# Kernel optimization log

Measured on AMD Instinct MI355X. Metric: run time of the kernel, lower is better.

## Reference

```python
import jax, jax.numpy as jnp
import numpy as np
import math

H, D, E, KD = 8, 128, 128, 16      # n_heads, input_dim, embed_dim, key_dim=val_dim
B, NPICK, NDEL = 16, 250, 250      # batch, pickups, deliveries per instance
G = 1 + NPICK + NDEL               # depot + picks + deliveries


def setup_inputs() -> dict:
    key = jax.random.key(0)
    ks = jax.random.split(key, 10)
    sk = 1.0 / math.sqrt(KD)
    se = 1.0 / math.sqrt(E)
    u = lambda k, shp, s: jax.random.uniform(k, shp, jnp.float32, -s, s)
    return {
        "q": jax.random.normal(ks[0], (B, G, D), jnp.float32),
        "W_query": u(ks[1], (H, D, KD), sk),
        "W_key": u(ks[2], (H, D, KD), sk),
        "W_val": u(ks[3], (H, D, KD), sk),
        "W1_query": u(ks[4], (H, D, KD), sk),
        "W2_query": u(ks[5], (H, D, KD), sk),
        "W3_query": u(ks[6], (H, D, KD), sk),
        "W4_query": u(ks[7], (H, D, KD), sk),
        "W_out": u(ks[8], (H, KD, E), se),
        "n_pick": NPICK,
        "n_delivery": NDEL,
    }


def reference(q, W_query, W_key, W_val, W1_query, W2_query, W3_query, W4_query,
              W_out, n_pick, n_delivery):
    h = q                                   # self-attention (h is None in caller)
    Bq, Gq, Dq = h.shape
    nh = W_query.shape[0]
    kd = W_query.shape[2]
    nf = 1.0 / math.sqrt(kd)
    NEG = jnp.float32(-jnp.inf)

    proj = lambda x, W: jnp.einsum('bnd,hdk->hbnk', x, W)   # (H,B,N,kd)
    scores = lambda Q, K: nf * jnp.einsum('hbqk,hbgk->hbqg', Q, K)
    # torch masked_fill_(x==0, -inf) on the group blocks (padding sentinel)
    zmask = lambda c: jnp.where(c == 0, NEG, c)

    Q = proj(q, W_query)
    K = proj(h, W_key)
    V = proj(h, W_val)
    comp = scores(Q, K)                      # (H,B,G,G)

    # split_embeddings: depot at 0, picks 1..n_pick, deliveries at the end
    hp = h[:, 1:1 + n_pick]                  # (B, n_pick, D)
    hd = h[:, 1 + n_pick:]                   # (B, n_delivery, D)

    Kp, Vp = proj(hp, W_key), proj(hp, W_val)
    Kd, Vd = proj(hd, W_key), proj(hd, W_val)

    c_pp = zmask(scores(proj(hp, W1_query), Kp))  # pick  -> all picks
    c_pd = zmask(scores(proj(hp, W2_query), Kd))  # pick  -> all deliveries
    c_dp = zmask(scores(proj(hd, W3_query), Kp))  # deliv -> all picks
    c_dd = zmask(scores(proj(hd, W4_query), Kd))  # deliv -> all deliveries

    def place(block, row_start):
        # scatter block rows into a (H,B,G,cols) tensor filled with -inf
        full = jnp.full((nh, Bq, Gq, block.shape[3]), NEG, dtype=block.dtype)
        return full.at[:, :, row_start:row_start + block.shape[2], :].set(block)

    add_pp = place(c_pp, 1)
    add_pd = place(c_pd, 1)
    add_dd = place(c_dd, Gq - n_delivery)
    add_dp = place(c_dp, Gq - n_delivery)

    comp_full = jnp.concatenate([comp, add_pp, add_pd, add_dd, add_dp], axis=-1)
    attn = jax.nn.softmax(comp_full, axis=-1)

    g, mp, md = Gq, n_pick, n_delivery
    heads = jnp.einsum('hbqg,hbgv->hbqv', attn[..., :g], V)
    heads = heads + jnp.einsum('hbqp,hbpv->hbqv', attn[..., g:g + mp], Vp)
    heads = heads + jnp.einsum('hbqd,hbdv->hbqv', attn[..., g + mp:g + mp + md], Vd)
    heads = heads + jnp.einsum('hbqd,hbdv->hbqv', attn[..., g + mp + md:g + mp + 2 * md], Vd)
    heads = heads + jnp.einsum('hbqp,hbpv->hbqv', attn[..., g + mp + 2 * md:g + 2 * mp + 2 * md], Vp)

    out = jnp.einsum('hbqv,hve->bqe', heads, W_out)   # (B, G, E)
    return out
```

## Files before the change

kernel.cpp:

```cpp
#include <hip/hip_runtime.h>
#include <math.h>

#define NH 8
#define DIM 128
#define KD 16
#define NB 16
#define NG 501
#define NPK 250
#define QROWS 512
#define QSCALE 0.36067376022224085f

typedef unsigned short ushort_t;
typedef __attribute__((ext_vector_type(8))) short short8v;
typedef __attribute__((ext_vector_type(4))) short short4v;
typedef __attribute__((ext_vector_type(2))) short short2v;
typedef __attribute__((ext_vector_type(4))) float f32x4;

#define MFMA(a, b, c) __builtin_amdgcn_mfma_f32_16x16x32_bf16(a, b, c, 0, 0, 0)

static __device__ __forceinline__ ushort_t f2bf(float x) {
  union { float f; unsigned u; } v; v.f = x;
  unsigned r = v.u + 0x7FFFu + ((v.u >> 16) & 1u);
  return (ushort_t)(r >> 16);
}
static __device__ __forceinline__ float bf2f(ushort_t h) {
  union { unsigned u; float f; } v; v.u = ((unsigned)h) << 16;
  return v.f;
}
static __device__ __forceinline__ unsigned cvtpk(float lo, float hi) {
  unsigned r;
  asm("v_cvt_pk_bf16_f32 %0, %1, %2" : "=v"(r) : "v"(lo), "v"(hi));
  return r;
}

__global__ __launch_bounds__(256) void conv_kernel(
    const float* __restrict__ q, ushort_t* __restrict__ qh,
    ushort_t* __restrict__ ql)
{
  int idx = blockIdx.x * 256 + threadIdx.x;
  int b  = idx >> 13;
  int r  = (idx >> 4) & 511;
  int c8 = (idx & 15) * 8;
  short8v h8 = {0,0,0,0,0,0,0,0}, l8 = {0,0,0,0,0,0,0,0};
  if (r < NG) {
    const float* src = &q[(size_t)(b * NG + r) * DIM + c8];
    float4 a = *(const float4*)src, d = *(const float4*)(src + 4);
    float vals[8] = {a.x, a.y, a.z, a.w, d.x, d.y, d.z, d.w};
#pragma unroll
    for (int j = 0; j < 8; ++j) {
      ushort_t hi = f2bf(vals[j]);
      h8[j] = (short)hi;
      l8[j] = (short)f2bf(vals[j] - bf2f(hi));
    }
  }
  size_t off = (size_t)(b * 512 + r) * DIM + c8;
  *(short8v*)&qh[off] = h8;
  *(short8v*)&ql[off] = l8;
}

__global__ __launch_bounds__(256) void proj_kernel(
    const ushort_t* __restrict__ qh_g, const ushort_t* __restrict__ ql_g,
    const float* __restrict__ wq, const float* __restrict__ wk,
    const float* __restrict__ wv, const float* __restrict__ w1,
    const float* __restrict__ w2, const float* __restrict__ w3,
    const float* __restrict__ w4,
    ushort_t* __restrict__ QcH, ushort_t* __restrict__ QcL,
    ushort_t* __restrict__ QPH, ushort_t* __restrict__ QPL,
    ushort_t* __restrict__ QDH, ushort_t* __restrict__ QDL,
    ushort_t* __restrict__ Kb,  ushort_t* __restrict__ Vt)
{
  const int rc = blockIdx.x, b = blockIdx.y, h = blockIdx.z;
  const int tid = threadIdx.x;
  const int wid = tid >> 6, lane = tid & 63;
  const int lrow = lane & 15, kgrp = lane >> 4;
  const size_t hb = (size_t)h * NB + b;

  const float* Wptr[7] = {wq, wk, wv, w1, w2, w3, w4};
  const int p0 = wid * 2;
  const int p1 = (wid < 3) ? wid * 2 + 1 : -1;

  short8v whf[2][4], wlf[2][4];
#pragma unroll
  for (int slot = 0; slot < 2; ++slot) {
    int p = slot ? p1 : p0;
    if (p < 0) continue;
    const float* W = Wptr[p] + h * 2048 + lrow;
#pragma unroll
    for (int c = 0; c < 4; ++c) {
      short8v hh, ll;
#pragma unroll
      for (int j = 0; j < 8; ++j) {
        float v = W[(c * 32 + kgrp * 8 + j) * 16];
        ushort_t hi = f2bf(v);
        hh[j] = (short)hi;
        ll[j] = (short)f2bf(v - bf2f(hi));
      }
      whf[slot][c] = hh; wlf[slot][c] = ll;
    }
  }

  const f32x4 zero4 = {0.f, 0.f, 0.f, 0.f};

#pragma unroll 1
  for (int iter = 0; iter < 2; ++iter) {
    const int rowbase = rc * 64 + iter * 32;
    short8v qhf[2][4], qlf[2][4];
#pragma unroll
    for (int s = 0; s < 2; ++s)
#pragma unroll
      for (int c = 0; c < 4; ++c) {
        size_t off = (size_t)(b * 512 + rowbase + s * 16 + lrow) * DIM + c * 32 + kgrp * 8;
        qhf[s][c] = *(const short8v*)(qh_g + off);
        qlf[s][c] = *(const short8v*)(ql_g + off);
      }

    f32x4 acc[2][2] = {{zero4, zero4}, {zero4, zero4}};
#pragma unroll
    for (int c = 0; c < 4; ++c)
#pragma unroll
      for (int slot = 0; slot < 2; ++slot) {
        int p = slot ? p1 : p0;
        if (p < 0) continue;
#pragma unroll
        for (int s = 0; s < 2; ++s) {
          if (p == 2) {
            acc[slot][s] = MFMA(whf[slot][c], qlf[s][c], acc[slot][s]);
            acc[slot][s] = MFMA(wlf[slot][c], qhf[s][c], acc[slot][s]);
            acc[slot][s] = MFMA(whf[slot][c], qhf[s][c], acc[slot][s]);
          } else {
            acc[slot][s] = MFMA(qlf[s][c], whf[slot][c], acc[slot][s]);
            acc[slot][s] = MFMA(qhf[s][c], wlf[slot][c], acc[slot][s]);
            acc[slot][s] = MFMA(qhf[s][c], whf[slot][c], acc[slot][s]);
          }
        }
      }

#pragma unroll
    for (int slot = 0; slot < 2; ++slot) {
      int p = slot ? p1 : p0;
      if (p < 0) continue;
#pragma unroll
      for (int s = 0; s < 2; ++s) {
#pragma unroll
        for (int rg = 0; rg < 4; ++rg) {
          float x = acc[slot][s][rg];
          if (p == 2) {
            int v = kgrp * 4 + rg;
            int g = rowbase + s * 16 + lrow;
            Vt[hb * 8192 + (size_t)v * 512 + g] = f2bf(x);
          } else {
            int row = rowbase + s * 16 + kgrp * 4 + rg;
            if (p == 0) {
              float xs = x * QSCALE;
              ushort_t hi = f2bf(xs), lo = f2bf(xs - bf2f(hi));
              size_t off = hb * 8192 + (size_t)row * 16 + lrow;
              QcH[off] = hi; QcL[off] = lo;
            } else if (p == 1) {
              ushort_t hi = f2bf(x), lo = f2bf(x - bf2f(hi));
              size_t off = hb * 16384 + (size_t)row * 32 + lrow;
              Kb[off] = hi; Kb[off + 16] = lo;
            } else {
              bool lowr = (p == 3 || p == 4);
              bool write = lowr ? (row <= NPK) : (row > NPK);
              if (write) {
                float xs = (row == 0) ? 0.f : x * QSCALE;
                ushort_t hi = f2bf(xs), lo = f2bf(xs - bf2f(hi));
                ushort_t* dH = (p == 3 || p == 5) ? QPH : QDH;
                ushort_t* dL = (p == 3 || p == 5) ? QPL : QDL;
                size_t off = hb * 8192 + (size_t)row * 16 + lrow;
                dH[off] = hi; dL[off] = lo;
              }
            }
          }
        }
      }
    }
  }
}

__global__ __launch_bounds__(256, 2) void attn_kernel(
    const ushort_t* __restrict__ QcH, const ushort_t* __restrict__ QcL,
    const ushort_t* __restrict__ QPH, const ushort_t* __restrict__ QPL,
    const ushort_t* __restrict__ QDH, const ushort_t* __restrict__ QDL,
    const ushort_t* __restrict__ Kb,  const ushort_t* __restrict__ Vt,
    ushort_t* __restrict__ HdH, ushort_t* __restrict__ HdL)
{
  __shared__ __align__(16) ushort_t Klds[16384];
  __shared__ __align__(16) ushort_t Vlds[8192];

  const int rt = blockIdx.x, b = blockIdx.y, h = blockIdx.z;
  const int tid = threadIdx.x;
  const int wid = tid >> 6, lane = tid & 63;
  const int lhalf = lane >> 4, lcol = lane & 15;
  const size_t hb = (size_t)h * NB + b;

  const ushort_t* Kg = Kb + hb * (size_t)(QROWS * 32);
  for (int c = tid; c < 2048; c += 256)
    *(short8v*)&Klds[c * 8] = *(const short8v*)(Kg + (size_t)c * 8);

  const ushort_t* Vg = Vt + hb * (size_t)(16 * QROWS);
#pragma unroll
  for (int it = 0; it < 4; ++it) {
    int c = it * 256 + tid;
    int blk = (it * 16) + (c & 15);
    int v = (c >> 4) & 15;
    int grp = blk >> 2, lh = blk & 3;
    short8v val = *(const short8v*)(Vg + (size_t)v * QROWS + blk * 8);
    *(short8v*)&Vlds[((grp * 4 + lh) * 16 + v) * 8] = val;
  }
  __syncthreads();

  const int wrow = rt * 128 + wid * 32;
  short8v qch[2], qcl[2], qph[2], qpl[2], qdh[2], qdl[2];
#pragma unroll
  for (int f = 0; f < 2; ++f) {
    int row = wrow + f * 16 + lcol;
    size_t off = hb * (size_t)(QROWS * 16) + (size_t)row * 16;
    size_t offh = off + (lhalf & 1) * 8;
    qch[f] = *(const short8v*)(QcH + offh);
    qph[f] = *(const short8v*)(QPH + offh);
    qdh[f] = *(const short8v*)(QDH + offh);
    short8v zl = {0,0,0,0,0,0,0,0};
    qcl[f] = zl; qpl[f] = zl; qdl[f] = zl;
    if (lhalf < 2) {
      size_t offl = off + lhalf * 8;
      qcl[f] = *(const short8v*)(QcL + offl);
      qpl[f] = *(const short8v*)(QPL + offl);
      qdl[f] = *(const short8v*)(QDL + offl);
    }
  }

  const f32x4 zero4 = {0.f, 0.f, 0.f, 0.f};
  f32x4 Oacc[2] = {zero4, zero4};
  float lsum[2] = {0.f, 0.f};
  const int srcA = ((lhalf & 1) * 2) * 16 + lcol;
  const int srcB = srcA + 16;
  const bool selhi = (lhalf >= 2);

#pragma unroll 1
  for (int grp = 0; grp < 16; ++grp) {
    float pv[2][2][4];
#pragma unroll
    for (int half = 0; half < 2; ++half) {
      const int ch = grp * 2 + half;
      short8v ka = *(const short8v*)&Klds[((ch * 16 + lcol) * 4 + lhalf) * 8];
#pragma unroll
      for (int qf = 0; qf < 2; ++qf) {
        f32x4 sc = MFMA(ka, qcl[qf], zero4);
        sc = MFMA(ka, qch[qf], sc);
        f32x4 se;
        if (ch == 15) {
          f32x4 sp = MFMA(ka, qpl[qf], zero4); sp = MFMA(ka, qph[qf], sp);
          f32x4 sd = MFMA(ka, qdl[qf], zero4); sd = MFMA(ka, qdh[qf], sd);
#pragma unroll
          for (int rg = 0; rg < 4; ++rg) {
            int key = 240 + lhalf * 4 + rg;
            se[rg] = (key <= NPK) ? sp[rg] : sd[rg];
          }
        } else if (ch <= 14) {
          se = MFMA(ka, qpl[qf], zero4); se = MFMA(ka, qph[qf], se);
        } else {
          se = MFMA(ka, qdl[qf], zero4); se = MFMA(ka, qdh[qf], se);
        }
#pragma unroll
        for (int rg = 0; rg < 4; ++rg) {
          float ec = __builtin_amdgcn_exp2f(sc[rg]);
          float ee = (se[rg] == 0.0f) ? 0.0f : __builtin_amdgcn_exp2f(se[rg]);
          if (ch == 0 && rg == 0) ee = (lhalf == 0) ? 0.0f : ee;
          float pt = ec + ee;
          if (ch == 31) pt = (lhalf * 4 + rg <= 4) ? pt : 0.0f;
          lsum[qf] += pt;
          pv[half][qf][rg] = pt;
        }
      }
    }
#pragma unroll
    for (int qf = 0; qf < 2; ++qf) {
      unsigned a0 = cvtpk(pv[0][qf][0], pv[0][qf][1]);
      unsigned a1 = cvtpk(pv[0][qf][2], pv[0][qf][3]);
      unsigned b0 = cvtpk(pv[1][qf][0], pv[1][qf][1]);
      unsigned b1 = cvtpk(pv[1][qf][2], pv[1][qf][3]);
      unsigned h0A = (unsigned)__shfl((int)a0, srcA);
      unsigned h0B = (unsigned)__shfl((int)a1, srcA);
      unsigned h0C = (unsigned)__shfl((int)a0, srcB);
      unsigned h0D = (unsigned)__shfl((int)a1, srcB);
      unsigned h1A = (unsigned)__shfl((int)b0, srcA);
      unsigned h1B = (unsigned)__shfl((int)b1, srcA);
      unsigned h1C = (unsigned)__shfl((int)b0, srcB);
      unsigned h1D = (unsigned)__shfl((int)b1, srcB);
      union { unsigned u[4]; short8v s; } pb;
      pb.u[0] = selhi ? h1A : h0A;
      pb.u[1] = selhi ? h1B : h0B;
      pb.u[2] = selhi ? h1C : h0C;
      pb.u[3] = selhi ? h1D : h0D;
      short8v va = *(const short8v*)&Vlds[((grp * 4 + lhalf) * 16 + lcol) * 8];
      Oacc[qf] = MFMA(va, pb.s, Oacc[qf]);
    }
  }

#pragma unroll
  for (int qf = 0; qf < 2; ++qf) {
    float l = lsum[qf];
    l += __shfl_xor(l, 16);
    l += __shfl_xor(l, 32);
    float inv = 1.0f / l;
    int row = wrow + qf * 16 + lcol;
    if (row < NG) {
      short4v ph, pl;
#pragma unroll
      for (int rg = 0; rg < 4; ++rg) {
        float o = Oacc[qf][rg] * inv;
        ushort_t hi = f2bf(o);
        ph[rg] = (short)hi;
        pl[rg] = (short)f2bf(o - bf2f(hi));
      }
      size_t off = (hb * 512 + (size_t)row) * 16 + lhalf * 4;
      *(short4v*)&HdH[off] = ph;
      *(short4v*)&HdL[off] = pl;
    }
  }
}

__global__ __launch_bounds__(256) void out_kernel(
    const ushort_t* __restrict__ HdH, const ushort_t* __restrict__ HdL,
    const float* __restrict__ Wout, float* __restrict__ out)
{
  const int eh = blockIdx.x, rt = blockIdx.y, b = blockIdx.z;
  const int tid = threadIdx.x;
  const int wid = tid >> 6, lane = tid & 63;
  const int lrow = lane & 15, kgrp = lane >> 4;
  const int e0 = eh * 64 + wid * 16 + lrow;

  short8v bh[4], bl[4];
#pragma unroll
  for (int c = 0; c < 4; ++c) {
    short8v hh, ll;
#pragma unroll
    for (int j = 0; j < 8; ++j) {
      float v = Wout[(size_t)(c * 32 + kgrp * 8 + j) * 128 + e0];
      ushort_t hi = f2bf(v);
      hh[j] = (short)hi;
      ll[j] = (short)f2bf(v - bf2f(hi));
    }
    bh[c] = hh; bl[c] = ll;
  }

  short8v ah[2][4], al[2][4];
#pragma unroll
  for (int s = 0; s < 2; ++s)
#pragma unroll
    for (int c = 0; c < 4; ++c) {
      int hh = (c * 4 + kgrp) >> 1, kd0 = ((c * 4 + kgrp) & 1) * 8;
      size_t off = ((size_t)(hh * NB + b) * 512 + rt * 32 + s * 16 + lrow) * 16 + kd0;
      ah[s][c] = *(const short8v*)(HdH + off);
      al[s][c] = *(const short8v*)(HdL + off);
    }

  const f32x4 zero4 = {0.f, 0.f, 0.f, 0.f};
  f32x4 acc[2] = {zero4, zero4};
#pragma unroll
  for (int c = 0; c < 4; ++c)
#pragma unroll
    for (int s = 0; s < 2; ++s) {
      acc[s] = MFMA(al[s][c], bh[c], acc[s]);
      acc[s] = MFMA(ah[s][c], bl[c], acc[s]);
      acc[s] = MFMA(ah[s][c], bh[c], acc[s]);
    }

#pragma unroll
  for (int s = 0; s < 2; ++s)
#pragma unroll
    for (int rg = 0; rg < 4; ++rg) {
      int g = rt * 32 + s * 16 + kgrp * 4 + rg;
      if (g < NG) out[((size_t)b * NG + g) * 128 + e0] = acc[s][rg];
    }
}

extern "C" void kernel_launch(void* const* d_in, const int* in_sizes, int n_in,
                              void* d_out, int out_size, void* d_ws, size_t ws_size,
                              hipStream_t stream)
{
  const float* q  = (const float*)d_in[0];
  const float* Wq = (const float*)d_in[1];
  const float* Wk = (const float*)d_in[2];
  const float* Wv = (const float*)d_in[3];
  const float* W1 = (const float*)d_in[4];
  const float* W2 = (const float*)d_in[5];
  const float* W3 = (const float*)d_in[6];
  const float* W4 = (const float*)d_in[7];
  const float* Wo = (const float*)d_in[8];
  float* out = (float*)d_out;

  char* wsb = (char*)d_ws;
  ushort_t* qh_g = (ushort_t*)(wsb + (0u  << 20));
  ushort_t* ql_g = (ushort_t*)(wsb + (2u  << 20));
  ushort_t* QcH  = (ushort_t*)(wsb + (4u  << 20));
  ushort_t* QcL  = (ushort_t*)(wsb + (6u  << 20));
  ushort_t* QPH  = (ushort_t*)(wsb + (8u  << 20));
  ushort_t* QPL  = (ushort_t*)(wsb + (10u << 20));
  ushort_t* QDH  = (ushort_t*)(wsb + (12u << 20));
  ushort_t* QDL  = (ushort_t*)(wsb + (14u << 20));
  ushort_t* Kb   = (ushort_t*)(wsb + (16u << 20));
  ushort_t* Vt   = (ushort_t*)(wsb + (20u << 20));
  ushort_t* HdH  = qh_g;
  ushort_t* HdL  = ql_g;

  conv_kernel<<<dim3(512), 256, 0, stream>>>(q, qh_g, ql_g);
  proj_kernel<<<dim3(8, NB, NH), 256, 0, stream>>>(qh_g, ql_g,
                                                   Wq, Wk, Wv, W1, W2, W3, W4,
                                                   QcH, QcL, QPH, QPL, QDH, QDL, Kb, Vt);
  attn_kernel<<<dim3(4, NB, NH), 256, 0, stream>>>(QcH, QcL, QPH, QPL, QDH, QDL,
                                                   Kb, Vt, HdH, HdL);
  out_kernel<<<dim3(2, 16, NB), 256, 0, stream>>>(HdH, HdL, Wo, out);
}
```

Measured before the change: 129.9 us.

## Fuse four stage kernels into one cooperative persistent kernel with grid syncs

Replaces the four separate launches (convert, project, attention, output) with a single cooperative kernel of 256 blocks of 512 threads that runs all stages and separates them with grid.sync. It also converts the weights to split bf16 hi/lo in a tile-friendly layout during the first stage, so later stages load pre-split fragments. The goal is to remove per-launch overhead and inter-kernel gaps. The cost is lower parallelism per stage (256 blocks), the grid barriers themselves, and more register pressure from the 512-thread blocks. The old multi-kernel path is kept as a fallback.

```diff
diff --git a/kernel.cpp b/kernel.cpp
--- a/kernel.cpp
+++ b/kernel.cpp
@@ -1,5 +1,8 @@
 #include <hip/hip_runtime.h>
+#include <hip/hip_cooperative_groups.h>
 #include <math.h>
+
+namespace cg = cooperative_groups;
 
 #define NH 8
 #define DIM 128
@@ -31,6 +34,357 @@
   unsigned r;
   asm("v_cvt_pk_bf16_f32 %0, %1, %2" : "=v"(r) : "v"(lo), "v"(hi));
   return r;
+}
+
+struct FArgs {
+  const float *q, *wq, *wk, *wv, *w1, *w2, *w3, *w4, *wo;
+  float* out;
+  char* ws;
+};
+
+
+__global__ __launch_bounds__(512, 2) void fused_kernel(FArgs a)
+{
+  __shared__ __align__(16) ushort_t Klds[16384];
+  __shared__ __align__(16) ushort_t Vlds[8192];
+
+  char* wsb = a.ws;
+  ushort_t* qh_g = (ushort_t*)(wsb + (0u  << 20));
+  ushort_t* ql_g = (ushort_t*)(wsb + (2u  << 20));
+  ushort_t* QcH  = (ushort_t*)(wsb + (4u  << 20));
+  ushort_t* QcL  = (ushort_t*)(wsb + (6u  << 20));
+  ushort_t* QPH  = (ushort_t*)(wsb + (8u  << 20));
+  ushort_t* QPL  = (ushort_t*)(wsb + (10u << 20));
+  ushort_t* QDH  = (ushort_t*)(wsb + (12u << 20));
+  ushort_t* QDL  = (ushort_t*)(wsb + (14u << 20));
+  ushort_t* Kb   = (ushort_t*)(wsb + (16u << 20));
+  ushort_t* Vt   = (ushort_t*)(wsb + (20u << 20));
+  ushort_t* Wsh  = (ushort_t*)(wsb + (22u << 20));
+  ushort_t* Wsl  = (ushort_t*)(wsb + (23u << 20));
+  ushort_t* Wosh = (ushort_t*)(wsb + (24u << 20));
+  ushort_t* Wosl = (ushort_t*)(wsb + (25u << 20));
+  ushort_t* HdH  = qh_g;
+  ushort_t* HdL  = ql_g;
+
+  cg::grid_group grid = cg::this_grid();
+  const int tid = threadIdx.x;
+  const int wid = tid >> 6, lane = tid & 63;
+
+  {
+    const int idx = blockIdx.x * 512 + tid;
+    {
+      int b = idx >> 13, r = (idx >> 4) & 511, c8 = (idx & 15) * 8;
+      short8v h8 = {0,0,0,0,0,0,0,0}, l8 = {0,0,0,0,0,0,0,0};
+      if (r < NG) {
+        const float* src = &a.q[(size_t)(b * NG + r) * DIM + c8];
+        float4 x = *(const float4*)src, y = *(const float4*)(src + 4);
+        float vals[8] = {x.x, x.y, x.z, x.w, y.x, y.y, y.z, y.w};
+#pragma unroll
+        for (int j = 0; j < 8; ++j) {
+          ushort_t hi = f2bf(vals[j]);
+          h8[j] = (short)hi;
+          l8[j] = (short)f2bf(vals[j] - bf2f(hi));
+        }
+      }
+      size_t off = (size_t)(b * 512 + r) * DIM + c8;
+      *(short8v*)&qh_g[off] = h8;
+      *(short8v*)&ql_g[off] = l8;
+    }
+    if (idx < 114688) {
+      int p = idx >> 14, rem = idx & 16383;
+      int h = rem >> 11, r2 = rem & 2047;
+      int d = r2 >> 4, lrow = r2 & 15;
+      const float* W = (p == 0) ? a.wq : (p == 1) ? a.wk : (p == 2) ? a.wv :
+                       (p == 3) ? a.w1 : (p == 4) ? a.w2 : (p == 5) ? a.w3 : a.w4;
+      float v = W[h * 2048 + d * 16 + lrow];
+      ushort_t hi = f2bf(v), lo = f2bf(v - bf2f(hi));
+      int c = d >> 5, kg = (d >> 3) & 3, j = d & 7;
+      size_t dst = ((((size_t)(p * 8 + h) * 4 + c) * 4 + kg) * 16 + lrow) * 8 + j;
+      Wsh[dst] = hi; Wsl[dst] = lo;
+    }
+    if (idx < 16384) {
+      int hkd = idx >> 7, e = idx & 127;
+      float v = a.wo[(size_t)hkd * 128 + e];
+      ushort_t hi = f2bf(v), lo = f2bf(v - bf2f(hi));
+      int c = hkd >> 5, kg = (hkd >> 3) & 3, j = hkd & 7;
+      size_t dst = (((size_t)c * 4 + kg) * 128 + e) * 8 + j;
+      Wosh[dst] = hi; Wosl[dst] = lo;
+    }
+  }
+  grid.sync();
+
+  {
+    const int lrow = lane & 15, kgrp = lane >> 4;
+    const int sub = wid >> 2, w4 = wid & 3;
+    const int p0 = w4 * 2;
+    const int p1 = (w4 < 3) ? w4 * 2 + 1 : -1;
+    const f32x4 zero4 = {0.f, 0.f, 0.f, 0.f};
+
+#pragma unroll 1
+    for (int u = 0; u < 2; ++u) {
+      const int unit = (blockIdx.x * 2 + sub) * 2 + u;
+      const int rc = unit & 7, b = (unit >> 3) & 15, h = unit >> 7;
+      const size_t hb = (size_t)h * NB + b;
+
+      short8v whf[2][4], wlf[2][4];
+#pragma unroll
+      for (int slot = 0; slot < 2; ++slot) {
+        int p = slot ? p1 : p0;
+        if (p < 0) continue;
+#pragma unroll
+        for (int c = 0; c < 4; ++c) {
+          size_t off = ((((size_t)(p * 8 + h) * 4 + c) * 4 + kgrp) * 16 + lrow) * 8;
+          whf[slot][c] = *(const short8v*)&Wsh[off];
+          wlf[slot][c] = *(const short8v*)&Wsl[off];
+        }
+      }
+
+#pragma unroll 1
+      for (int iter = 0; iter < 2; ++iter) {
+        const int rowbase = rc * 64 + iter * 32;
+        short8v qhf[2][4], qlf[2][4];
+#pragma unroll
+        for (int s = 0; s < 2; ++s)
+#pragma unroll
+          for (int c = 0; c < 4; ++c) {
+            size_t off = (size_t)(b * 512 + rowbase + s * 16 + lrow) * DIM + c * 32 + kgrp * 8;
+            qhf[s][c] = *(const short8v*)(qh_g + off);
+            qlf[s][c] = *(const short8v*)(ql_g + off);
+          }
+
+        f32x4 acc[2][2] = {{zero4, zero4}, {zero4, zero4}};
+#pragma unroll
+        for (int c = 0; c < 4; ++c)
+#pragma unroll
+          for (int slot = 0; slot < 2; ++slot) {
+            int p = slot ? p1 : p0;
+            if (p < 0) continue;
+#pragma unroll
+            for (int s = 0; s < 2; ++s) {
+              if (p == 2) {
+                acc[slot][s] = MFMA(whf[slot][c], qlf[s][c], acc[slot][s]);
+                acc[slot][s] = MFMA(wlf[slot][c], qhf[s][c], acc[slot][s]);
+                acc[slot][s] = MFMA(whf[slot][c], qhf[s][c], acc[slot][s]);
+              } else {
+                acc[slot][s] = MFMA(qlf[s][c], whf[slot][c], acc[slot][s]);
+                acc[slot][s] = MFMA(qhf[s][c], wlf[slot][c], acc[slot][s]);
+                acc[slot][s] = MFMA(qhf[s][c], whf[slot][c], acc[slot][s]);
+              }
+            }
+          }
+
+#pragma unroll
+        for (int slot = 0; slot < 2; ++slot) {
+          int p = slot ? p1 : p0;
+          if (p < 0) continue;
+#pragma unroll
+          for (int s = 0; s < 2; ++s) {
+#pragma unroll
+            for (int rg = 0; rg < 4; ++rg) {
+              float x = acc[slot][s][rg];
+              if (p == 2) {
+                int v = kgrp * 4 + rg;
+                int g = rowbase + s * 16 + lrow;
+                Vt[hb * 8192 + (size_t)v * 512 + g] = f2bf(x);
+              } else {
+                int row = rowbase + s * 16 + kgrp * 4 + rg;
+                if (p == 0) {
+                  float xs = x * QSCALE;
+                  ushort_t hi = f2bf(xs), lo = f2bf(xs - bf2f(hi));
+                  size_t off = hb * 8192 + (size_t)row * 16 + lrow;
+                  QcH[off] = hi; QcL[off] = lo;
+                } else if (p == 1) {
+                  ushort_t hi = f2bf(x), lo = f2bf(x - bf2f(hi));
+                  size_t off = hb * 16384 + (size_t)row * 32 + lrow;
+                  Kb[off] = hi; Kb[off + 16] = lo;
+                } else {
+                  bool lowr = (p == 3 || p == 4);
+                  bool write = lowr ? (row <= NPK) : (row > NPK);
+                  if (write) {
+                    float xs = (row == 0) ? 0.f : x * QSCALE;
+                    ushort_t hi = f2bf(xs), lo = f2bf(xs - bf2f(hi));
+                    ushort_t* dH = (p == 3 || p == 5) ? QPH : QDH;
+                    ushort_t* dL = (p == 3 || p == 5) ? QPL : QDL;
+                    size_t off = hb * 8192 + (size_t)row * 16 + lrow;
+                    dH[off] = hi; dL[off] = lo;
+                  }
+                }
+              }
+            }
+          }
+        }
+      }
+    }
+  }
+  grid.sync();
+
+  {
+    const int lhalf = lane >> 4, lcol = lane & 15;
+    const int srcA = ((lhalf & 1) * 2) * 16 + lcol;
+    const int srcB = srcA + 16;
+    const bool selhi = (lhalf >= 2);
+    const f32x4 zero4 = {0.f, 0.f, 0.f, 0.f};
+
+#pragma unroll 1
+    for (int tt = 0; tt < 2; ++tt) {
+      const int tile = blockIdx.x * 2 + tt;
+      const int rt = tile & 3, b = (tile >> 2) & 15, h = tile >> 6;
+      const size_t hb = (size_t)h * NB + b;
+
+      const ushort_t* Kg = Kb + hb * (size_t)(QROWS * 32);
+      for (int c = tid; c < 2048; c += 512)
+        *(short8v*)&Klds[c * 8] = *(const short8v*)(Kg + (size_t)c * 8);
+
+      const ushort_t* Vg = Vt + hb * (size_t)(16 * QROWS);
+#pragma unroll
+      for (int it = 0; it < 2; ++it) {
+        int i = it * 512 + tid;
+        int v = (i >> 4) & 15;
+        int blk = (i >> 8) * 16 + (i & 15);
+        int g2 = blk >> 2, lh = blk & 3;
+        short8v val = *(const short8v*)(Vg + (size_t)v * QROWS + blk * 8);
+        *(short8v*)&Vlds[((g2 * 4 + lh) * 16 + v) * 8] = val;
+      }
+      __syncthreads();
+
+      const int wrow = rt * 128 + wid * 16;
+      const int row = wrow + lcol;
+      size_t off = hb * (size_t)(QROWS * 16) + (size_t)row * 16;
+      size_t offh = off + (lhalf & 1) * 8;
+      short8v qch = *(const short8v*)(QcH + offh);
+      short8v qph = *(const short8v*)(QPH + offh);
+      short8v qdh = *(const short8v*)(QDH + offh);
+      short8v qcl = {0,0,0,0,0,0,0,0}, qpl = qcl, qdl = qcl;
+      if (lhalf < 2) {
+        size_t offl = off + lhalf * 8;
+        qcl = *(const short8v*)(QcL + offl);
+        qpl = *(const short8v*)(QPL + offl);
+        qdl = *(const short8v*)(QDL + offl);
+      }
+
+      f32x4 Oacc = zero4;
+      float lsum = 0.f;
+
+#pragma unroll 1
+      for (int grp = 0; grp < 16; ++grp) {
+        float pv[2][4];
+#pragma unroll
+        for (int half = 0; half < 2; ++half) {
+          const int ch = grp * 2 + half;
+          short8v ka = *(const short8v*)&Klds[((ch * 16 + lcol) * 4 + lhalf) * 8];
+          f32x4 sc = MFMA(ka, qcl, zero4);
+          sc = MFMA(ka, qch, sc);
+          f32x4 se;
+          if (ch == 15) {
+            f32x4 sp = MFMA(ka, qpl, zero4); sp = MFMA(ka, qph, sp);
+            f32x4 sd = MFMA(ka, qdl, zero4); sd = MFMA(ka, qdh, sd);
+#pragma unroll
+            for (int rg = 0; rg < 4; ++rg) {
+              int key = 240 + lhalf * 4 + rg;
+              se[rg] = (key <= NPK) ? sp[rg] : sd[rg];
+            }
+          } else if (ch <= 14) {
+            se = MFMA(ka, qpl, zero4); se = MFMA(ka, qph, se);
+          } else {
+            se = MFMA(ka, qdl, zero4); se = MFMA(ka, qdh, se);
+          }
+#pragma unroll
+          for (int rg = 0; rg < 4; ++rg) {
+            float ec = __builtin_amdgcn_exp2f(sc[rg]);
+            float ee = (se[rg] == 0.0f) ? 0.0f : __builtin_amdgcn_exp2f(se[rg]);
+            if (ch == 0 && rg == 0) ee = (lhalf == 0) ? 0.0f : ee;
+            float pt = ec + ee;
+            if (ch == 31) pt = (lhalf * 4 + rg <= 4) ? pt : 0.0f;
+            lsum += pt;
+            pv[half][rg] = pt;
+          }
+        }
+        unsigned a0 = cvtpk(pv[0][0], pv[0][1]);
+        unsigned a1 = cvtpk(pv[0][2], pv[0][3]);
+        unsigned b0 = cvtpk(pv[1][0], pv[1][1]);
+        unsigned b1 = cvtpk(pv[1][2], pv[1][3]);
+        unsigned h0A = (unsigned)__shfl((int)a0, srcA);
+        unsigned h0B = (unsigned)__shfl((int)a1, srcA);
+        unsigned h0C = (unsigned)__shfl((int)a0, srcB);
+        unsigned h0D = (unsigned)__shfl((int)a1, srcB);
+        unsigned h1A = (unsigned)__shfl((int)b0, srcA);
+        unsigned h1B = (unsigned)__shfl((int)b1, srcA);
+        unsigned h1C = (unsigned)__shfl((int)b0, srcB);
+        unsigned h1D = (unsigned)__shfl((int)b1, srcB);
+        union { unsigned u[4]; short8v s; } pb;
+        pb.u[0] = selhi ? h1A : h0A;
+        pb.u[1] = selhi ? h1B : h0B;
+        pb.u[2] = selhi ? h1C : h0C;
+        pb.u[3] = selhi ? h1D : h0D;
+        short8v va = *(const short8v*)&Vlds[((grp * 4 + lhalf) * 16 + lcol) * 8];
+        Oacc = MFMA(va, pb.s, Oacc);
+      }
+
+      float l = lsum;
+      l += __shfl_xor(l, 16);
+      l += __shfl_xor(l, 32);
+      float inv = 1.0f / l;
+      if (row < NG) {
+        short4v ph, pl;
+#pragma unroll
+        for (int rg = 0; rg < 4; ++rg) {
+          float o = Oacc[rg] * inv;
+          ushort_t hi = f2bf(o);
+          ph[rg] = (short)hi;
+          pl[rg] = (short)f2bf(o - bf2f(hi));
+        }
+        size_t doff = (hb * 512 + (size_t)row) * 16 + lhalf * 4;
+        *(short4v*)&HdH[doff] = ph;
+        *(short4v*)&HdL[doff] = pl;
+      }
+      __syncthreads();
+    }
+  }
+  grid.sync();
+
+  {
+    const int rt = blockIdx.x & 15, b = blockIdx.x >> 4;
+    const int lrow = lane & 15, kgrp = lane >> 4;
+    const int e0 = wid * 16 + lrow;
+
+    short8v bh[4], bl[4];
+#pragma unroll
+    for (int c = 0; c < 4; ++c) {
+      size_t off = (((size_t)c * 4 + kgrp) * 128 + e0) * 8;
+      bh[c] = *(const short8v*)&Wosh[off];
+      bl[c] = *(const short8v*)&Wosl[off];
+    }
+
+    short8v ah[2][4], al[2][4];
+#pragma unroll
+    for (int s = 0; s < 2; ++s)
+#pragma unroll
+      for (int c = 0; c < 4; ++c) {
+        int hh = (c * 4 + kgrp) >> 1, kd0 = ((c * 4 + kgrp) & 1) * 8;
+        size_t off = ((size_t)(hh * NB + b) * 512 + rt * 32 + s * 16 + lrow) * 16 + kd0;
+        ah[s][c] = *(const short8v*)(HdH + off);
+        al[s][c] = *(const short8v*)(HdL + off);
+      }
+
+    const f32x4 zero4 = {0.f, 0.f, 0.f, 0.f};
+    f32x4 acc[2] = {zero4, zero4};
+#pragma unroll
+    for (int c = 0; c < 4; ++c)
+#pragma unroll
+      for (int s = 0; s < 2; ++s) {
+        acc[s] = MFMA(al[s][c], bh[c], acc[s]);
+        acc[s] = MFMA(ah[s][c], bl[c], acc[s]);
+        acc[s] = MFMA(ah[s][c], bh[c], acc[s]);
+      }
+
+#pragma unroll
+    for (int s = 0; s < 2; ++s)
+#pragma unroll
+      for (int rg = 0; rg < 4; ++rg) {
+        int g = rt * 32 + s * 16 + kgrp * 4 + rg;
+        if (g < NG) a.out[((size_t)b * NG + g) * 128 + e0] = acc[s][rg];
+      }
+  }
 }
 
 __global__ __launch_bounds__(256) void conv_kernel(
@@ -204,9 +558,9 @@
     int c = it * 256 + tid;
     int blk = (it * 16) + (c & 15);
     int v = (c >> 4) & 15;
-    int grp = blk >> 2, lh = blk & 3;
+    int g2 = blk >> 2, lh = blk & 3;
     short8v val = *(const short8v*)(Vg + (size_t)v * QROWS + blk * 8);
-    *(short8v*)&Vlds[((grp * 4 + lh) * 16 + v) * 8] = val;
+    *(short8v*)&Vlds[((g2 * 4 + lh) * 16 + v) * 8] = val;
   }
   __syncthreads();
 
@@ -380,36 +734,49 @@
                               void* d_out, int out_size, void* d_ws, size_t ws_size,
                               hipStream_t stream)
 {
-  const float* q  = (const float*)d_in[0];
-  const float* Wq = (const float*)d_in[1];
-  const float* Wk = (const float*)d_in[2];
-  const float* Wv = (const float*)d_in[3];
-  const float* W1 = (const float*)d_in[4];
-  const float* W2 = (const float*)d_in[5];
-  const float* W3 = (const float*)d_in[6];
-  const float* W4 = (const float*)d_in[7];
-  const float* Wo = (const float*)d_in[8];
-  float* out = (float*)d_out;
-
-  char* wsb = (char*)d_ws;
-  ushort_t* qh_g = (ushort_t*)(wsb + (0u  << 20));
-  ushort_t* ql_g = (ushort_t*)(wsb + (2u  << 20));
-  ushort_t* QcH  = (ushort_t*)(wsb + (4u  << 20));
-  ushort_t* QcL  = (ushort_t*)(wsb + (6u  << 20));
-  ushort_t* QPH  = (ushort_t*)(wsb + (8u  << 20));
-  ushort_t* QPL  = (ushort_t*)(wsb + (10u << 20));
-  ushort_t* QDH  = (ushort_t*)(wsb + (12u << 20));
-  ushort_t* QDL  = (ushort_t*)(wsb + (14u << 20));
-  ushort_t* Kb   = (ushort_t*)(wsb + (16u << 20));
-  ushort_t* Vt   = (ushort_t*)(wsb + (20u << 20));
-  ushort_t* HdH  = qh_g;
-  ushort_t* HdL  = ql_g;
-
-  conv_kernel<<<dim3(512), 256, 0, stream>>>(q, qh_g, ql_g);
-  proj_kernel<<<dim3(8, NB, NH), 256, 0, stream>>>(qh_g, ql_g,
-                                                   Wq, Wk, Wv, W1, W2, W3, W4,
-                                                   QcH, QcL, QPH, QPL, QDH, QDL, Kb, Vt);
-  attn_kernel<<<dim3(4, NB, NH), 256, 0, stream>>>(QcH, QcL, QPH, QPL, QDH, QDL,
-                                                   Kb, Vt, HdH, HdL);
-  out_kernel<<<dim3(2, 16, NB), 256, 0, stream>>>(HdH, HdL, Wo, out);
-}
+  FArgs a;
+  a.q  = (const float*)d_in[0];
+  a.wq = (const float*)d_in[1];
+  a.wk = (const float*)d_in[2];
+  a.wv = (const float*)d_in[3];
+  a.w1 = (const float*)d_in[4];
+  a.w2 = (const float*)d_in[5];
+  a.w3 = (const float*)d_in[6];
+  a.w4 = (const float*)d_in[7];
+  a.wo = (const float*)d_in[8];
+  a.out = (float*)d_out;
+  a.ws  = (char*)d_ws;
+
+  bool done = false;
+  int nb = 0;
+  hipError_t qe = hipOccupancyMaxActiveBlocksPerMultiprocessor(&nb, fused_kernel, 512, 0);
+  if (qe == hipSuccess && nb >= 1) {
+    void* kp[] = {&a};
+    hipError_t le = hipLaunchCooperativeKernel(fused_kernel, dim3(256), dim3(512), kp, 0, stream);
+    done = (le == hipSuccess);
+  }
+
+  if (!done) {
+    char* wsb = (char*)d_ws;
+    ushort_t* qh_g = (ushort_t*)(wsb + (0u  << 20));
+    ushort_t* ql_g = (ushort_t*)(wsb + (2u  << 20));
+    ushort_t* QcH  = (ushort_t*)(wsb + (4u  << 20));
+    ushort_t* QcL  = (ushort_t*)(wsb + (6u  << 20));
+    ushort_t* QPH  = (ushort_t*)(wsb + (8u  << 20));
+    ushort_t* QPL  = (ushort_t*)(wsb + (10u << 20));
+    ushort_t* QDH  = (ushort_t*)(wsb + (12u << 20));
+    ushort_t* QDL  = (ushort_t*)(wsb + (14u << 20));
+    ushort_t* Kb   = (ushort_t*)(wsb + (16u << 20));
+    ushort_t* Vt   = (ushort_t*)(wsb + (20u << 20));
+    ushort_t* HdH  = qh_g;
+    ushort_t* HdL  = ql_g;
+
+    conv_kernel<<<dim3(512), 256, 0, stream>>>(a.q, qh_g, ql_g);
+    proj_kernel<<<dim3(8, NB, NH), 256, 0, stream>>>(qh_g, ql_g,
+                                                     a.wq, a.wk, a.wv, a.w1, a.w2, a.w3, a.w4,
+                                                     QcH, QcL, QPH, QPL, QDH, QDL, Kb, Vt);
+    attn_kernel<<<dim3(4, NB, NH), 256, 0, stream>>>(QcH, QcL, QPH, QPL, QDH, QDL,
+                                                     Kb, Vt, HdH, HdL);
+    out_kernel<<<dim3(2, 16, NB), 256, 0, stream>>>(HdH, HdL, a.wo, out_size ? (float*)d_out : nullptr);
+  }
+}
```

Result: no change. 130.2 us (+0.2%).
